# Kernel tuning notes

Hardware: AMD Instinct MI355X
Metric: run time of the kernel (lower is better)

## Reference

```python
import jax, jax.numpy as jnp
import numpy as np

E, QE, P, H = 3, 60000, 40, 20   # elements, atoms per element, fp length, hidden
NIMG = 1800                       # images in batch
Q = E * QE                        # total atoms
NNZ = 14_400_000                  # nnz of sparse fprimes [P*Q, 3*Q]


def setup_inputs() -> dict:
    key = jax.random.key(0)
    ks = jax.random.split(key, 12)
    fps = jax.random.normal(ks[0], (E, QE, P), jnp.float32)
    image_idx = jax.random.randint(ks[1], (E, QE), 0, NIMG, jnp.int32)
    s1 = 1.0 / np.sqrt(P)
    s2 = 1.0 / np.sqrt(H)
    W1 = (jax.random.normal(ks[2], (E, P, H)) * s1).astype(jnp.float32)
    b1 = jnp.zeros((E, H), jnp.float32)
    W2 = (jax.random.normal(ks[3], (E, H, H)) * s2).astype(jnp.float32)
    b2 = jnp.zeros((E, H), jnp.float32)
    W3 = (jax.random.normal(ks[4], (E, H, 1)) * s2).astype(jnp.float32)
    b3 = jnp.zeros((E, 1), jnp.float32)
    fp_rows = jax.random.randint(ks[5], (NNZ,), 0, P * Q, jnp.int32)
    fp_cols = jax.random.randint(ks[6], (NNZ,), 0, 3 * Q, jnp.int32)
    fp_vals = (jax.random.normal(ks[7], (NNZ,)) * 0.05).astype(jnp.float32)
    return {"fps": fps, "W1": W1, "b1": b1, "W2": W2, "b2": b2, "W3": W3,
            "b3": b3, "image_idx": image_idx, "fp_rows": fp_rows,
            "fp_cols": fp_cols, "fp_vals": fp_vals, "batch_size": NIMG}


def _mlp(x, w1, b1, w2, b2, w3, b3):
    # Dense(tanh) -> Dense(tanh) -> Dense(linear), per amptorch MLP(n_layers=3)
    h = jnp.tanh(x @ w1 + b1)
    h = jnp.tanh(h @ w2 + b2)
    return h @ w3 + b3  # [..., 1]


def _esum(x, w1, b1, w2, b2, w3, b3):
    return _mlp(x, w1, b1, w2, b2, w3, b3).sum()


def reference(fps, W1, b1, W2, b2, W3, b3, image_idx, fp_rows, fp_cols,
              fp_vals, batch_size):
    # per-element atomwise energies: [E, QE, 1]
    atom_e = jax.vmap(_mlp)(fps, W1, b1, W2, b2, W3, b3)
    # scatter-add atomic energies into per-image energies (index_add_)
    energy_pred = jax.ops.segment_sum(
        atom_e.reshape(-1, 1), image_idx.reshape(-1).astype(jnp.int32),
        num_segments=batch_size)  # [NIMG, 1]
    # dE/dFP per atom (each atom's output depends only on its own fp, so
    # grad of the per-element energy sum == per-atom jacobian rows)
    dE_dFP = jax.vmap(jax.grad(_esum))(fps, W1, b1, W2, b2, W3, b3)  # [E,QE,P]
    # reorder atoms from element-grouped order to image-index order
    # (stable argsort == boolean-match reorder in the torch code)
    order = jnp.argsort(image_idx.reshape(-1))
    dE_flat = dE_dFP.reshape(-1, P)[order].reshape(-1)  # [P*Q]
    # force = -fprimes^T @ dE_dFP  (sparse COO matvec via segment_sum)
    force_flat = -jax.ops.segment_sum(
        fp_vals * dE_flat[fp_rows], fp_cols, num_segments=3 * Q)
    force_pred = force_flat.reshape(-1, 3)  # [Q, 3]
    return energy_pred, force_pred
```

## Files before the change

kernel.cpp:

```cpp
#include <hip/hip_runtime.h>
#include <math.h>

#define E_    3
#define QE_   60000
#define QTOT  180000
#define P_    40
#define H_    20
#define NIMG_ 1800
#define NNZ_  14400000
#define BLK   256
#define NB    704

#define CW_BITS 12
#define CW      4096
#define NBIN    132
#define SUBS    8
#define SC      8192
#define NSB     1758

#define SLICE_SHIFT 17
#define NSLICE  55

#define GSPLIT  4
#define NREG    220
#define CAPS4   68096
#define NCH4    2048
#define NGMAX   384
#define FS_GRID 1792
#define FS_PERX 224

#define C_SCUR  0
#define C_GCNT  256
#define C_NCH   264
#define C_CHID  512
#define C_GRP   2560
#define C_INTS  5632

typedef int   vi4 __attribute__((ext_vector_type(4)));
typedef float vf4 __attribute__((ext_vector_type(4)));
typedef unsigned uint32;

__global__ void zero_kernel(float* __restrict__ out, int n) {
    int i = blockIdx.x * blockDim.x + threadIdx.x;
    if (i < n) out[i] = 0.0f;
}
__global__ void zero_ctrl_kernel(int* __restrict__ ctrl) {
    ctrl[threadIdx.x] = 0;
}

__global__ void hist_kernel(const int* __restrict__ img, int* __restrict__ g_hist) {
    __shared__ int h[NIMG_];
    const int t = threadIdx.x, b = blockIdx.x;
    for (int v = t; v < NIMG_; v += BLK) h[v] = 0;
    __syncthreads();
    int a = b * BLK + t;
    if (a < QTOT) atomicAdd(&h[img[a]], 1);
    __syncthreads();
    for (int v = t; v < NIMG_; v += BLK) g_hist[v * NB + b] = h[v];
}

__global__ void scan_blocks_kernel(int* __restrict__ g_hist, int* __restrict__ g_total) {
    __shared__ int s[BLK];
    const int v = blockIdx.x, t = threadIdx.x;
    int carry = 0;
    for (int c = 0; c < NB; c += BLK) {
        int idx = c + t;
        int val = (idx < NB) ? g_hist[v * NB + idx] : 0;
        s[t] = val; __syncthreads();
        for (int off = 1; off < BLK; off <<= 1) {
            int tmp = (t >= off) ? s[t - off] : 0;
            __syncthreads();
            s[t] += tmp;
            __syncthreads();
        }
        int excl = s[t] - val;
        int tot  = s[BLK - 1];
        if (idx < NB) g_hist[v * NB + idx] = carry + excl;
        carry += tot;
        __syncthreads();
    }
    if (t == 0) g_total[v] = carry;
}

__global__ void scan_buckets_kernel(const int* __restrict__ g_total, int* __restrict__ g_base) {
    __shared__ int s[BLK];
    const int t = threadIdx.x;
    int carry = 0;
    for (int c = 0; c < NIMG_; c += BLK) {
        int idx = c + t;
        int val = (idx < NIMG_) ? g_total[idx] : 0;
        s[t] = val; __syncthreads();
        for (int off = 1; off < BLK; off <<= 1) {
            int tmp = (t >= off) ? s[t - off] : 0;
            __syncthreads();
            s[t] += tmp;
            __syncthreads();
        }
        if (idx < NIMG_) g_base[idx] = carry + (s[t] - val);
        carry += s[BLK - 1];
        __syncthreads();
    }
}

__global__ void rank_kernel(const int* __restrict__ img, const int* __restrict__ g_hist,
                            const int* __restrict__ g_base, int* __restrict__ rank) {
    __shared__ int simg[BLK];
    const int t = threadIdx.x, b = blockIdx.x;
    int a = b * BLK + t;
    int v = (a < QTOT) ? img[a] : -1;
    simg[t] = v;
    __syncthreads();
    if (a < QTOT) {
        int local = 0;
        for (int j = 0; j < t; ++j) {
            if (simg[j] == v) local++;
        }
        rank[a] = g_base[v] + g_hist[v * NB + b] + local;
    }
}

__global__ __launch_bounds__(BLK) void mlp_kernel(
    const float* __restrict__ fps, const float* __restrict__ W1, const float* __restrict__ b1,
    const float* __restrict__ W2, const float* __restrict__ b2, const float* __restrict__ W3,
    const float* __restrict__ b3, const int* __restrict__ img, const int* __restrict__ rank,
    float* __restrict__ energy, float* __restrict__ dEflat)
{
    __shared__ float sW1[P_ * H_], sW2[H_ * H_], sW3[H_], sB1[H_], sB2[H_];
    __shared__ float sB3;
    const int e = blockIdx.y;
    const int t = threadIdx.x;
    for (int i = t; i < P_ * H_; i += BLK) sW1[i] = W1[e * P_ * H_ + i];
    for (int i = t; i < H_ * H_; i += BLK) sW2[i] = W2[e * H_ * H_ + i];
    if (t < H_) { sW3[t] = W3[e * H_ + t]; sB1[t] = b1[e * H_ + t]; sB2[t] = b2[e * H_ + t]; }
    if (t == 0) sB3 = b3[e];
    __syncthreads();

    int q = blockIdx.x * BLK + t;
    if (q >= QE_) return;
    int a = e * QE_ + q;

    const vf4* xp = (const vf4*)(fps + (size_t)a * P_);
    float x[P_];
    #pragma unroll
    for (int p = 0; p < P_; p += 4) {
        vf4 v4 = __builtin_nontemporal_load(xp + (p >> 2));
        x[p] = v4.x; x[p+1] = v4.y; x[p+2] = v4.z; x[p+3] = v4.w;
    }

    float h1v[H_], h2v[H_];
    #pragma unroll
    for (int i = 0; i < H_; ++i) {
        float z = sB1[i];
        #pragma unroll
        for (int p = 0; p < P_; ++p) z += x[p] * sW1[p * H_ + i];
        h1v[i] = tanhf(z);
    }
    #pragma unroll
    for (int i = 0; i < H_; ++i) {
        float z = sB2[i];
        #pragma unroll
        for (int j = 0; j < H_; ++j) z += h1v[j] * sW2[j * H_ + i];
        h2v[i] = tanhf(z);
    }
    float ea = sB3;
    #pragma unroll
    for (int i = 0; i < H_; ++i) ea += h2v[i] * sW3[i];
    atomicAdd(&energy[img[a]], ea);

    float dz2[H_];
    #pragma unroll
    for (int i = 0; i < H_; ++i) dz2[i] = sW3[i] * (1.0f - h2v[i] * h2v[i]);
    float dz1[H_];
    #pragma unroll
    for (int i = 0; i < H_; ++i) {
        float d = 0.0f;
        #pragma unroll
        for (int j = 0; j < H_; ++j) d += sW2[i * H_ + j] * dz2[j];
        dz1[i] = d * (1.0f - h1v[i] * h1v[i]);
    }
    float* op = dEflat + (size_t)rank[a] * P_;
    #pragma unroll
    for (int p = 0; p < P_; p += 4) {
        float4 v4;
        float d0 = 0.f, d1 = 0.f, d2 = 0.f, d3 = 0.f;
        #pragma unroll
        for (int i = 0; i < H_; ++i) {
            d0 += sW1[(p    ) * H_ + i] * dz1[i];
            d1 += sW1[(p + 1) * H_ + i] * dz1[i];
            d2 += sW1[(p + 2) * H_ + i] * dz1[i];
            d3 += sW1[(p + 3) * H_ + i] * dz1[i];
        }
        v4.x = d0; v4.y = d1; v4.z = d2; v4.w = d3;
        *(float4*)(op + p) = v4;
    }
}

__global__ __launch_bounds__(BLK) void slice_scatter_kernel(
    const int* __restrict__ rows, const int* __restrict__ cols, const float* __restrict__ vals,
    int* __restrict__ ctrl, uint2* __restrict__ items)
{
    __shared__ uint32 srow[SC];
    __shared__ int h[NSLICE], lcur[NSLICE], gbase[NSLICE];
    const int t = threadIdx.x, b = blockIdx.x;
    const int g = b & (GSPLIT - 1);
    const int base = b * SC;
    const int len = min(SC, NNZ_ - base);
    const bool full = (len == SC);

    if (t < NSLICE) h[t] = 0;
    __syncthreads();
    if (full) {
        const vi4* r4 = (const vi4*)(rows + base);
        #pragma unroll
        for (int j = 0; j < SC / (BLK * 4); ++j) {
            int idx = j * BLK + t;
            vi4 rr = __builtin_nontemporal_load(r4 + idx);
            srow[idx * 4 + 0] = (uint32)rr.x; atomicAdd(&h[rr.x >> SLICE_SHIFT], 1);
            srow[idx * 4 + 1] = (uint32)rr.y; atomicAdd(&h[rr.y >> SLICE_SHIFT], 1);
            srow[idx * 4 + 2] = (uint32)rr.z; atomicAdd(&h[rr.z >> SLICE_SHIFT], 1);
            srow[idx * 4 + 3] = (uint32)rr.w; atomicAdd(&h[rr.w >> SLICE_SHIFT], 1);
        }
    } else {
        for (int j = t; j < len; j += BLK) {
            int r = rows[base + j];
            srow[j] = (uint32)r;
            atomicAdd(&h[r >> SLICE_SHIFT], 1);
        }
    }
    __syncthreads();
    if (t < NSLICE) {
        lcur[t] = 0;
        gbase[t] = (h[t] > 0) ? atomicAdd(&ctrl[C_SCUR + g * NSLICE + t], h[t]) : 0;
    }
    __syncthreads();
    if (full) {
        const vi4* c4 = (const vi4*)(cols + base);
        const vi4* v4 = (const vi4*)(vals + base);
        #pragma unroll 2
        for (int j = 0; j < SC / (BLK * 4); ++j) {
            int idx = j * BLK + t;
            vi4 cc = __builtin_nontemporal_load(c4 + idx);
            vi4 vv = __builtin_nontemporal_load(v4 + idx);
            #define EMIT(K, CI, VB)                                                \
            {                                                                      \
                uint32 r = srow[idx * 4 + K];                                      \
                int sl = (int)(r >> SLICE_SHIFT);                                  \
                int pos = gbase[sl] + atomicAdd(&lcur[sl], 1);                     \
                uint32 v15 = (((uint32)(VB)) + 0x10000u) >> 17;                    \
                items[(size_t)(g * NSLICE + sl) * CAPS4 + pos] =                   \
                    make_uint2((v15 << 17) | (r & 0x1FFFFu), (uint32)(CI));        \
            }
            EMIT(0, cc.x, vv.x)
            EMIT(1, cc.y, vv.y)
            EMIT(2, cc.z, vv.z)
            EMIT(3, cc.w, vv.w)
        }
    } else {
        for (int j = t; j < len; j += BLK) {
            uint32 r = srow[j];
            int sl = (int)(r >> SLICE_SHIFT);
            int pos = gbase[sl] + atomicAdd(&lcur[sl], 1);
            uint32 vb = ((const uint32*)vals)[base + j];
            uint32 v15 = (vb + 0x10000u) >> 17;
            items[(size_t)(g * NSLICE + sl) * CAPS4 + pos] =
                make_uint2((v15 << 17) | (r & 0x1FFFFu), (uint32)cols[base + j]);
        }
    }
}

__global__ void plan4_kernel(int* __restrict__ ctrl) {
    __shared__ int nc[NREG];
    const int t = threadIdx.x;
    if (t < NREG) {
        int cnt = ctrl[C_SCUR + t];
        nc[t] = (cnt + SC - 1) / SC;
    }
    __syncthreads();
    if (t < NREG) {
        const int myx = (t % NSLICE) & 7;
        int cb = 0, gp = 0;
        for (int g2 = 0; g2 < t; ++g2) {
            int v = nc[g2];
            cb += v;
            if (((g2 % NSLICE) & 7) == myx) gp += v;
        }
        const int myn = nc[t];
        for (int c = 0; c < myn; ++c) {
            ctrl[C_CHID + cb + c] = (t << 8) | c;
            ctrl[C_GRP + myx * NGMAX + gp + c] = cb + c;
        }
    }
    if (t < 8) {
        int s = 0;
        for (int g2 = 0; g2 < NREG; ++g2)
            if (((g2 % NSLICE) & 7) == t) s += nc[g2];
        ctrl[C_GCNT + t] = s;
    }
    if (t == 0) {
        int tot = 0;
        for (int g2 = 0; g2 < NREG; ++g2) tot += nc[g2];
        ctrl[C_NCH] = tot;
    }
}

__global__ __launch_bounds__(BLK) void fhist4_kernel(
    const uint2* __restrict__ items, const int* __restrict__ ctrl,
    int* __restrict__ binHist, unsigned short* __restrict__ binCnt)
{
    __shared__ int h[NBIN];
    const int t = threadIdx.x, j = blockIdx.x;
    const int tot = ctrl[C_NCH];
    if (t < NBIN) h[t] = 0;
    __syncthreads();
    if (j < tot) {
        const int pkd = ctrl[C_CHID + j];
        const int gi = pkd >> 8, c = pkd & 255;
        const int start = gi * CAPS4 + c * SC;
        const int len = min(SC, ctrl[C_SCUR + gi] - c * SC);
        if (len == SC) {
            const vi4* p4 = (const vi4*)(items + start);
            #pragma unroll
            for (int k = 0; k < SC / (BLK * 2); ++k) {
                vi4 q = __builtin_nontemporal_load(p4 + k * BLK + t);
                atomicAdd(&h[((uint32)q.y) >> CW_BITS], 1);
                atomicAdd(&h[((uint32)q.w) >> CW_BITS], 1);
            }
        } else {
            for (int k = t; k < len; k += BLK)
                atomicAdd(&h[items[start + k].y >> CW_BITS], 1);
        }
    }
    __syncthreads();
    if (t < NBIN) {
        binHist[t * NCH4 + j] = h[t];
        binCnt[t * NCH4 + j] = (unsigned short)h[t];
    }
}

__global__ void fscan_blocks_kernel(int* __restrict__ binHist, int* __restrict__ binTotal,
                                    int n) {
    __shared__ int s[BLK];
    const int v = blockIdx.x, t = threadIdx.x;
    int carry = 0;
    for (int c = 0; c < n; c += BLK) {
        int idx = c + t;
        int val = (idx < n) ? binHist[v * n + idx] : 0;
        s[t] = val; __syncthreads();
        for (int off = 1; off < BLK; off <<= 1) {
            int tmp = (t >= off) ? s[t - off] : 0;
            __syncthreads();
            s[t] += tmp;
            __syncthreads();
        }
        int excl = s[t] - val;
        int tot  = s[BLK - 1];
        if (idx < n) binHist[v * n + idx] = carry + excl;
        carry += tot;
        __syncthreads();
    }
    if (t == 0) binTotal[v] = carry;
}

__global__ void fbase_kernel(const int* __restrict__ binTotal, int* __restrict__ binBase) {
    __shared__ int s[BLK];
    const int t = threadIdx.x;
    int v = (t < NBIN) ? binTotal[t] : 0;
    s[t] = v; __syncthreads();
    for (int off = 1; off < BLK; off <<= 1) {
        int tmp = (t >= off) ? s[t - off] : 0;
        __syncthreads();
        s[t] += tmp;
        __syncthreads();
    }
    if (t < NBIN) binBase[t] = s[t] - v;
    if (t == 0) binBase[NBIN] = s[BLK - 1];
}

__global__ __launch_bounds__(BLK) void fscatter4_kernel(
    const uint2* __restrict__ items, const float* __restrict__ dEflat,
    const int* __restrict__ ctrl, const int* __restrict__ binHist,
    const unsigned short* __restrict__ binCnt, const int* __restrict__ binBase,
    uint32* __restrict__ bm)
{
    __shared__ uint32 itl[SC];
    __shared__ unsigned char bns[SC];
    __shared__ int cur[NBIN], dlt[NBIN];
    __shared__ int sc[BLK];
    const int t = threadIdx.x;
    const int x = blockIdx.x & 7;
    const int r = blockIdx.x >> 3;
    const int gc = ctrl[C_GCNT + x];

    for (int w = r; w < gc; w += FS_PERX) {
        const int j     = ctrl[C_GRP + x * NGMAX + w];
        const int pkd   = ctrl[C_CHID + j];
        const int gi    = pkd >> 8;
        const int c     = pkd & 255;
        const int start = gi * CAPS4 + c * SC;
        const int len   = min(SC, ctrl[C_SCUR + gi] - c * SC);
        const int sl    = gi % NSLICE;
        const float* __restrict__ dE = dEflat + ((size_t)sl << SLICE_SHIFT);

        {
            int v = (t < NBIN) ? (int)binCnt[t * NCH4 + j] : 0;
            sc[t] = v; __syncthreads();
            for (int off = 1; off < BLK; off <<= 1) {
                int tmp = (t >= off) ? sc[t - off] : 0;
                __syncthreads();
                sc[t] += tmp;
                __syncthreads();
            }
            if (t < NBIN) {
                int st = sc[t] - v;
                cur[t] = st;
                dlt[t] = binBase[t] + binHist[t * NCH4 + j] - st;
            }
        }
        __syncthreads();
        #define PLACE4(LO, CO, DI)                                             \
        {                                                                      \
            uint32 col = (uint32)(CO);                                         \
            int bin = (int)(col >> CW_BITS);                                   \
            float val = __uint_as_float((((uint32)(LO)) >> 17) << 17);         \
            uint32 u = __float_as_uint(-val * (DI));                           \
            uint32 pk = ((col & (CW - 1)) << 20) | ((u + 0x800u) >> 12);       \
            int pos = atomicAdd(&cur[bin], 1);                                 \
            itl[pos] = pk;                                                     \
            bns[pos] = (unsigned char)bin;                                     \
        }
        if (len == SC) {
            const vi4* p4 = (const vi4*)(items + start);
            #pragma unroll 4
            for (int k = 0; k < SC / (BLK * 2); ++k) {
                vi4 q = __builtin_nontemporal_load(p4 + k * BLK + t);
                float dA = dE[((uint32)q.x) & 0x1FFFFu];
                float dB = dE[((uint32)q.z) & 0x1FFFFu];
                PLACE4(q.x, q.y, dA)
                PLACE4(q.z, q.w, dB)
            }
        } else {
            for (int k = t; k < len; k += BLK) {
                uint2 it = items[start + k];
                float d = dE[it.x & 0x1FFFFu];
                PLACE4(it.x, it.y, d)
            }
        }
        __syncthreads();
        for (int i = t; i < len; i += BLK) {
            __builtin_nontemporal_store(itl[i], &bm[dlt[bns[i]] + i]);
        }
        __syncthreads();
    }
}

__global__ __launch_bounds__(BLK) void fforce_kernel(
    const uint32* __restrict__ bm, const int* __restrict__ binBase,
    float* __restrict__ partial)
{
    __shared__ float w[CW];
    const int t = threadIdx.x;
    const int bin = blockIdx.x >> 3;
    const int sub = blockIdx.x & (SUBS - 1);
    for (int i = t; i < CW; i += BLK) w[i] = 0.0f;
    __syncthreads();
    const int start = binBase[bin];
    const int cnt   = binBase[bin + 1] - start;
    const int sBeg  = start + (cnt * sub) / SUBS;
    const int sEnd  = start + (cnt * (sub + 1)) / SUBS;
    int i = sBeg + t;
    for (; i + 3 * BLK < sEnd; i += 4 * BLK) {
        uint32 p0 = __builtin_nontemporal_load(bm + i);
        uint32 p1 = __builtin_nontemporal_load(bm + i + BLK);
        uint32 p2 = __builtin_nontemporal_load(bm + i + 2 * BLK);
        uint32 p3 = __builtin_nontemporal_load(bm + i + 3 * BLK);
        atomicAdd(&w[p0 >> 20], __uint_as_float((p0 & 0xFFFFFu) << 12));
        atomicAdd(&w[p1 >> 20], __uint_as_float((p1 & 0xFFFFFu) << 12));
        atomicAdd(&w[p2 >> 20], __uint_as_float((p2 & 0xFFFFFu) << 12));
        atomicAdd(&w[p3 >> 20], __uint_as_float((p3 & 0xFFFFFu) << 12));
    }
    for (; i < sEnd; i += BLK) {
        uint32 p = bm[i];
        atomicAdd(&w[p >> 20], __uint_as_float((p & 0xFFFFFu) << 12));
    }
    __syncthreads();
    float* dst = partial + (size_t)blockIdx.x * CW;
    for (int k = t; k < CW; k += BLK) __builtin_nontemporal_store(w[k], dst + k);
}

__global__ void freduce_kernel(const float* __restrict__ partial, float* __restrict__ force) {
    int i = blockIdx.x * BLK + threadIdx.x;
    if (i < 3 * QTOT) {
        int bin = i >> CW_BITS, local = i & (CW - 1);
        const float* p = partial + (size_t)bin * (CW * SUBS) + local;
        float sum = 0.0f;
        #pragma unroll
        for (int k = 0; k < SUBS; ++k) sum += __builtin_nontemporal_load(p + k * CW);
        force[i] = sum;
    }
}

__global__ void force_kernel(const int* __restrict__ rows, const int* __restrict__ cols,
                             const float* __restrict__ vals, const float* __restrict__ dEflat,
                             float* __restrict__ force) {
    int k = blockIdx.x * blockDim.x + threadIdx.x;
    if (k < NNZ_) {
        float contrib = -vals[k] * dEflat[rows[k]];
        atomicAdd(&force[cols[k]], contrib);
    }
}

extern "C" void kernel_launch(void* const* d_in, const int* in_sizes, int n_in,
                              void* d_out, int out_size, void* d_ws, size_t ws_size,
                              hipStream_t stream) {
    (void)in_sizes; (void)n_in; (void)out_size;
    const float* fps  = (const float*)d_in[0];
    const float* W1   = (const float*)d_in[1];
    const float* b1   = (const float*)d_in[2];
    const float* W2   = (const float*)d_in[3];
    const float* b2   = (const float*)d_in[4];
    const float* W3   = (const float*)d_in[5];
    const float* b3   = (const float*)d_in[6];
    const int*   img  = (const int*)d_in[7];
    const int*   rows = (const int*)d_in[8];
    const int*   cols = (const int*)d_in[9];
    const float* vals = (const float*)d_in[10];

    char* ws = (char*)d_ws;
    float* energy = (float*)d_out;
    float* force  = (float*)d_out + NIMG_;
    const int nOut = NIMG_ + 3 * QTOT;

    int*    g_hist   = (int*)(ws);
    int*    g_total  = (int*)(ws + 5068800);
    int*    g_base   = (int*)(ws + 5076000);
    int*    rank     = (int*)(ws + 5083200);
    uint2*  items    = (uint2*)(ws);
    float*  partial4 = (float*)(ws);
    uint32* bm4      = (uint32*)(ws + 119848960);
    int*    binHist  = (int*)(ws + 177448960);
    unsigned short* binCnt = (unsigned short*)(ws + 178530304);
    int*    binTotal = (int*)(ws + 179070976);
    int*    binBase  = (int*)(ws + 179071504);
    int*    ctrl     = (int*)(ws + 179072064);
    float*  dEflat4  = (float*)(ws + 179536384);
    const size_t WS_V4 = 208336384;

    float*  dEflat5 = (float*)(ws + 5803200);
    const size_t WS_MIN = 5803200 + (size_t)QTOT * P_ * 4;

    const bool v4 = (ws_size >= WS_V4);
    float* dEflat = v4 ? dEflat4 : dEflat5;

    zero_kernel<<<(nOut + BLK - 1) / BLK, BLK, 0, stream>>>((float*)d_out, nOut);

    hist_kernel<<<NB, BLK, 0, stream>>>(img, g_hist);
    scan_blocks_kernel<<<NIMG_, BLK, 0, stream>>>(g_hist, g_total);
    scan_buckets_kernel<<<1, BLK, 0, stream>>>(g_total, g_base);
    rank_kernel<<<NB, BLK, 0, stream>>>(img, g_hist, g_base, rank);

    dim3 gm((QE_ + BLK - 1) / BLK, E_);
    mlp_kernel<<<gm, BLK, 0, stream>>>(fps, W1, b1, W2, b2, W3, b3, img, rank,
                                       energy, dEflat);

    if (v4) {
        zero_ctrl_kernel<<<1, 512, 0, stream>>>(ctrl);
        slice_scatter_kernel<<<NSB, BLK, 0, stream>>>(rows, cols, vals, ctrl, items);
        plan4_kernel<<<1, BLK, 0, stream>>>(ctrl);
        fhist4_kernel<<<NCH4, BLK, 0, stream>>>(items, ctrl, binHist, binCnt);
        fscan_blocks_kernel<<<NBIN, BLK, 0, stream>>>(binHist, binTotal, NCH4);
        fbase_kernel<<<1, BLK, 0, stream>>>(binTotal, binBase);
        fscatter4_kernel<<<FS_GRID, BLK, 0, stream>>>(items, dEflat, ctrl,
                                                      binHist, binCnt, binBase, bm4);
        fforce_kernel<<<NBIN * SUBS, BLK, 0, stream>>>(bm4, binBase, partial4);
        freduce_kernel<<<(3 * QTOT + BLK - 1) / BLK, BLK, 0, stream>>>(partial4, force);
    } else if (ws_size >= WS_MIN) {
        force_kernel<<<NNZ_ / BLK, BLK, 0, stream>>>(rows, cols, vals, dEflat, force);
    }
}
```

Baseline: 613.3 us.

## Fuse bin histogram into scatter and use fixed-capacity bins with atomic cursors

Removes the separate per-chunk histogram, block scan and base-scan kernels. The scatter kernel now builds its chunk's column-bin histogram in shared memory and reserves output space with global atomics on per-bin cursors inside fixed-capacity bin regions (CAPB). The force kernel reads bin counts from those cursors. It also drops the nontemporal load/store hints, changes the scatter unroll from 4 to 2, and skips zeroing the force output on the v4 path. The cost is that each chunk is read twice inside the scatter kernel and the bin order becomes nondeterministic. There is also an overflow risk if any bin exceeds its fixed capacity.

```diff
diff --git a/kernel.cpp b/kernel.cpp
--- a/kernel.cpp
+++ b/kernel.cpp
@@ -17,21 +17,23 @@
 #define SUBS    8
 #define SC      8192
 #define NSB     1758
+#define CAPB    114688
 
 #define SLICE_SHIFT 17
 #define NSLICE  55
 
 #define GSPLIT  4
 #define NREG    220
-#define CAPS4   68096
+#define CAPS4   67584
 #define NCH4    2048
 #define NGMAX   384
 #define FS_GRID 1792
 #define FS_PERX 224
 
 #define C_SCUR  0
-#define C_GCNT  256
-#define C_NCH   264
+#define C_BCUR  224
+#define C_GCNT  360
+#define C_NCH   368
 #define C_CHID  512
 #define C_GRP   2560
 #define C_INTS  5632
@@ -303,88 +305,13 @@
     }
 }
 
-__global__ __launch_bounds__(BLK) void fhist4_kernel(
-    const uint2* __restrict__ items, const int* __restrict__ ctrl,
-    int* __restrict__ binHist, unsigned short* __restrict__ binCnt)
-{
-    __shared__ int h[NBIN];
-    const int t = threadIdx.x, j = blockIdx.x;
-    const int tot = ctrl[C_NCH];
-    if (t < NBIN) h[t] = 0;
-    __syncthreads();
-    if (j < tot) {
-        const int pkd = ctrl[C_CHID + j];
-        const int gi = pkd >> 8, c = pkd & 255;
-        const int start = gi * CAPS4 + c * SC;
-        const int len = min(SC, ctrl[C_SCUR + gi] - c * SC);
-        if (len == SC) {
-            const vi4* p4 = (const vi4*)(items + start);
-            #pragma unroll
-            for (int k = 0; k < SC / (BLK * 2); ++k) {
-                vi4 q = __builtin_nontemporal_load(p4 + k * BLK + t);
-                atomicAdd(&h[((uint32)q.y) >> CW_BITS], 1);
-                atomicAdd(&h[((uint32)q.w) >> CW_BITS], 1);
-            }
-        } else {
-            for (int k = t; k < len; k += BLK)
-                atomicAdd(&h[items[start + k].y >> CW_BITS], 1);
-        }
-    }
-    __syncthreads();
-    if (t < NBIN) {
-        binHist[t * NCH4 + j] = h[t];
-        binCnt[t * NCH4 + j] = (unsigned short)h[t];
-    }
-}
-
-__global__ void fscan_blocks_kernel(int* __restrict__ binHist, int* __restrict__ binTotal,
-                                    int n) {
-    __shared__ int s[BLK];
-    const int v = blockIdx.x, t = threadIdx.x;
-    int carry = 0;
-    for (int c = 0; c < n; c += BLK) {
-        int idx = c + t;
-        int val = (idx < n) ? binHist[v * n + idx] : 0;
-        s[t] = val; __syncthreads();
-        for (int off = 1; off < BLK; off <<= 1) {
-            int tmp = (t >= off) ? s[t - off] : 0;
-            __syncthreads();
-            s[t] += tmp;
-            __syncthreads();
-        }
-        int excl = s[t] - val;
-        int tot  = s[BLK - 1];
-        if (idx < n) binHist[v * n + idx] = carry + excl;
-        carry += tot;
-        __syncthreads();
-    }
-    if (t == 0) binTotal[v] = carry;
-}
-
-__global__ void fbase_kernel(const int* __restrict__ binTotal, int* __restrict__ binBase) {
-    __shared__ int s[BLK];
-    const int t = threadIdx.x;
-    int v = (t < NBIN) ? binTotal[t] : 0;
-    s[t] = v; __syncthreads();
-    for (int off = 1; off < BLK; off <<= 1) {
-        int tmp = (t >= off) ? s[t - off] : 0;
-        __syncthreads();
-        s[t] += tmp;
-        __syncthreads();
-    }
-    if (t < NBIN) binBase[t] = s[t] - v;
-    if (t == 0) binBase[NBIN] = s[BLK - 1];
-}
-
 __global__ __launch_bounds__(BLK) void fscatter4_kernel(
     const uint2* __restrict__ items, const float* __restrict__ dEflat,
-    const int* __restrict__ ctrl, const int* __restrict__ binHist,
-    const unsigned short* __restrict__ binCnt, const int* __restrict__ binBase,
-    uint32* __restrict__ bm)
+    int* __restrict__ ctrl, uint32* __restrict__ bm)
 {
     __shared__ uint32 itl[SC];
     __shared__ unsigned char bns[SC];
-    __shared__ int cur[NBIN], dlt[NBIN];
+    __shared__ int h[NBIN], cur[NBIN], dlt[NBIN];
     __shared__ int sc[BLK];
     const int t = threadIdx.x;
     const int x = blockIdx.x & 7;
@@ -401,8 +328,23 @@
         const int sl    = gi % NSLICE;
         const float* __restrict__ dE = dEflat + ((size_t)sl << SLICE_SHIFT);
 
+        if (t < NBIN) h[t] = 0;
+        __syncthreads();
+        if (len == SC) {
+            const vi4* p4 = (const vi4*)(items + start);
+            #pragma unroll
+            for (int k = 0; k < SC / (BLK * 2); ++k) {
+                vi4 q = p4[k * BLK + t];
+                atomicAdd(&h[((uint32)q.y) >> CW_BITS], 1);
+                atomicAdd(&h[((uint32)q.w) >> CW_BITS], 1);
+            }
+        } else {
+            for (int k = t; k < len; k += BLK)
+                atomicAdd(&h[items[start + k].y >> CW_BITS], 1);
+        }
+        __syncthreads();
         {
-            int v = (t < NBIN) ? (int)binCnt[t * NCH4 + j] : 0;
+            int v = (t < NBIN) ? h[t] : 0;
             sc[t] = v; __syncthreads();
             for (int off = 1; off < BLK; off <<= 1) {
                 int tmp = (t >= off) ? sc[t - off] : 0;
@@ -411,9 +353,10 @@
                 __syncthreads();
             }
             if (t < NBIN) {
-                int st = sc[t] - v;
-                cur[t] = st;
-                dlt[t] = binBase[t] + binHist[t * NCH4 + j] - st;
+                int ls = sc[t] - v;
+                cur[t] = ls;
+                int gb = (v > 0) ? atomicAdd(&ctrl[C_BCUR + t], v) : 0;
+                dlt[t] = t * CAPB + gb - ls;
             }
         }
         __syncthreads();
@@ -430,9 +373,9 @@
         }
         if (len == SC) {
             const vi4* p4 = (const vi4*)(items + start);
-            #pragma unroll 4
+            #pragma unroll 2
             for (int k = 0; k < SC / (BLK * 2); ++k) {
-                vi4 q = __builtin_nontemporal_load(p4 + k * BLK + t);
+                vi4 q = p4[k * BLK + t];
                 float dA = dE[((uint32)q.x) & 0x1FFFFu];
                 float dB = dE[((uint32)q.z) & 0x1FFFFu];
                 PLACE4(q.x, q.y, dA)
@@ -447,14 +390,14 @@
         }
         __syncthreads();
         for (int i = t; i < len; i += BLK) {
-            __builtin_nontemporal_store(itl[i], &bm[dlt[bns[i]] + i]);
+            bm[dlt[bns[i]] + i] = itl[i];
         }
         __syncthreads();
     }
 }
 
 __global__ __launch_bounds__(BLK) void fforce_kernel(
-    const uint32* __restrict__ bm, const int* __restrict__ binBase,
+    const uint32* __restrict__ bm, const int* __restrict__ ctrl,
     float* __restrict__ partial)
 {
     __shared__ float w[CW];
@@ -463,16 +406,16 @@
     const int sub = blockIdx.x & (SUBS - 1);
     for (int i = t; i < CW; i += BLK) w[i] = 0.0f;
     __syncthreads();
-    const int start = binBase[bin];
-    const int cnt   = binBase[bin + 1] - start;
+    const int cnt   = ctrl[C_BCUR + bin];
+    const int start = bin * CAPB;
     const int sBeg  = start + (cnt * sub) / SUBS;
     const int sEnd  = start + (cnt * (sub + 1)) / SUBS;
     int i = sBeg + t;
     for (; i + 3 * BLK < sEnd; i += 4 * BLK) {
-        uint32 p0 = __builtin_nontemporal_load(bm + i);
-        uint32 p1 = __builtin_nontemporal_load(bm + i + BLK);
-        uint32 p2 = __builtin_nontemporal_load(bm + i + 2 * BLK);
-        uint32 p3 = __builtin_nontemporal_load(bm + i + 3 * BLK);
+        uint32 p0 = bm[i];
+        uint32 p1 = bm[i + BLK];
+        uint32 p2 = bm[i + 2 * BLK];
+        uint32 p3 = bm[i + 3 * BLK];
         atomicAdd(&w[p0 >> 20], __uint_as_float((p0 & 0xFFFFFu) << 12));
         atomicAdd(&w[p1 >> 20], __uint_as_float((p1 & 0xFFFFFu) << 12));
         atomicAdd(&w[p2 >> 20], __uint_as_float((p2 & 0xFFFFFu) << 12));
@@ -536,12 +479,8 @@
     int*    rank     = (int*)(ws + 5083200);
     uint2*  items    = (uint2*)(ws);
     float*  partial4 = (float*)(ws);
-    uint32* bm4      = (uint32*)(ws + 119848960);
-    int*    binHist  = (int*)(ws + 177448960);
-    unsigned short* binCnt = (unsigned short*)(ws + 178530304);
-    int*    binTotal = (int*)(ws + 179070976);
-    int*    binBase  = (int*)(ws + 179071504);
-    int*    ctrl     = (int*)(ws + 179072064);
+    uint32* bm4      = (uint32*)(ws + 118947840);
+    int*    ctrl     = (int*)(ws + 179503104);
     float*  dEflat4  = (float*)(ws + 179536384);
     const size_t WS_V4 = 208336384;
 
@@ -551,7 +490,11 @@
     const bool v4 = (ws_size >= WS_V4);
     float* dEflat = v4 ? dEflat4 : dEflat5;
 
-    zero_kernel<<<(nOut + BLK - 1) / BLK, BLK, 0, stream>>>((float*)d_out, nOut);
+    if (v4) {
+        zero_kernel<<<(NIMG_ + BLK - 1) / BLK, BLK, 0, stream>>>(energy, NIMG_);
+    } else {
+        zero_kernel<<<(nOut + BLK - 1) / BLK, BLK, 0, stream>>>((float*)d_out, nOut);
+    }
 
     hist_kernel<<<NB, BLK, 0, stream>>>(img, g_hist);
     scan_blocks_kernel<<<NIMG_, BLK, 0, stream>>>(g_hist, g_total);
@@ -566,12 +509,8 @@
         zero_ctrl_kernel<<<1, 512, 0, stream>>>(ctrl);
         slice_scatter_kernel<<<NSB, BLK, 0, stream>>>(rows, cols, vals, ctrl, items);
         plan4_kernel<<<1, BLK, 0, stream>>>(ctrl);
-        fhist4_kernel<<<NCH4, BLK, 0, stream>>>(items, ctrl, binHist, binCnt);
-        fscan_blocks_kernel<<<NBIN, BLK, 0, stream>>>(binHist, binTotal, NCH4);
-        fbase_kernel<<<1, BLK, 0, stream>>>(binTotal, binBase);
-        fscatter4_kernel<<<FS_GRID, BLK, 0, stream>>>(items, dEflat, ctrl,
-                                                      binHist, binCnt, binBase, bm4);
-        fforce_kernel<<<NBIN * SUBS, BLK, 0, stream>>>(bm4, binBase, partial4);
+        fscatter4_kernel<<<FS_GRID, BLK, 0, stream>>>(items, dEflat, ctrl, bm4);
+        fforce_kernel<<<NBIN * SUBS, BLK, 0, stream>>>(bm4, ctrl, partial4);
         freduce_kernel<<<(3 * QTOT + BLK - 1) / BLK, BLK, 0, stream>>>(partial4, force);
     } else if (ws_size >= WS_MIN) {
         force_kernel<<<NNZ_ / BLK, BLK, 0, stream>>>(rows, cols, vals, dEflat, force);
```

Measured after the change: 592.4 us. 1.04x faster.
